# Kernel tuning notes

Hardware: AMD Instinct MI355X
Metric: run time of the kernel (lower is better)

The kernel has to match this reference:

```python
import jax, jax.numpy as jnp
import numpy as np

B, L, H = 8, 128, 768
VOCAB, FEAT_VOCAB, NUM_LABELS = 30522, 16384, 3


def setup_inputs() -> dict:
    key = jax.random.key(0)
    ks = jax.random.split(key, 12)
    return {
        "sequence_output": jax.random.normal(ks[0], (B, L, H), jnp.float32),
        "pooled_output": jax.random.normal(ks[1], (B, H), jnp.float32),
        "W_key": jax.random.normal(ks[2], (VOCAB, H), jnp.float32) * 0.02,
        "W_val": jax.random.normal(ks[3], (FEAT_VOCAB, H), jnp.float32) * 0.02,
        "W_dense": jax.random.normal(ks[4], (NUM_LABELS, 2 * H), jnp.float32) * 0.02,
        "b_dense": jnp.zeros((NUM_LABELS,), jnp.float32),
        "valid_ids": jax.random.randint(ks[5], (B, L), 0, 2, jnp.int32),
        "text_kv_indices": jax.random.randint(ks[6], (B, L), 0, VOCAB, jnp.int64 if jax.config.jax_enable_x64 else jnp.int32),
        "features": jax.random.randint(ks[7], (B, L, L), 0, FEAT_VOCAB, jnp.int64 if jax.config.jax_enable_x64 else jnp.int32),
        "pos_matrix": jax.random.randint(ks[8], (B, L, L), 0, 2, jnp.int32),
        "aspect_indices": jax.random.randint(ks[9], (B, L), 0, 2, jnp.int32),
    }


def reference(sequence_output, pooled_output, W_key, W_val, W_dense, b_dense,
              valid_ids, text_kv_indices, features, pos_matrix, aspect_indices):
    b, l, h = sequence_output.shape
    # --- vectorized valid-token pack (replaces per-sample python loop) ---
    # stable argsort puts valid (==1) token positions first, in order
    order = jnp.argsort(1 - valid_ids, axis=1, stable=True)          # [B,L]
    gathered = jnp.take_along_axis(sequence_output, order[:, :, None], axis=1)
    count = valid_ids.sum(axis=1)                                    # [B]
    keep = jnp.arange(l)[None, :] < count[:, None]                   # [B,L]
    valid_output = gathered * keep[:, :, None].astype(jnp.float32)
    asp = aspect_indices[:, :, None].astype(jnp.float32)             # [B,L,1]
    hidden = valid_output * asp
    # --- KeyValueMemoryNetwork ---
    Wk = W_key.at[0].set(0.0)   # padding_idx=0
    Wv = W_val.at[0].set(0.0)   # padding_idx=0
    key_embed = Wk[text_kv_indices]                                  # [B,L,H]
    value_embed = Wv[features]                                       # [B,L,L,H]
    scale = jnp.float32(np.power(h, 0.5))
    u = jnp.einsum('bqh,bkh->bqk', hidden, key_embed) / scale        # [B,L,L]
    delta = jnp.exp(u) * pos_matrix.astype(jnp.float32)
    p = delta / (delta.sum(axis=2, keepdims=True) + 1e-10)           # [B,L,L]
    o = jnp.einsum('bqk,bqkh->bqh', p, value_embed)                  # [B,L,H]
    aspect_len = (o != 0).sum(axis=1).astype(jnp.float32)            # [B,H]
    avg_o = o.sum(axis=1) / aspect_len                               # [B,H]
    # --- head (incro == 'cat'; dropout is identity at eval) ---
    c = jnp.concatenate([pooled_output, avg_o], axis=1)              # [B,2H]
    logits = c @ W_dense.T + b_dense                                 # [B,3]
    return logits
```

## Files before the change

### kernel.cpp

```cpp
#include <hip/hip_runtime.h>

#define NB 8
#define SL 128
#define HD 768

typedef float v2f __attribute__((ext_vector_type(2)));

__device__ __forceinline__ float bf_lo(unsigned int u) {
  return __uint_as_float(u << 16);
}
__device__ __forceinline__ float bf_hi(unsigned int u) {
  return __uint_as_float(u & 0xffff0000u);
}
__device__ __forceinline__ unsigned short f2bf(float x) {
  unsigned int b = __float_as_uint(x);
  b += 0x7fffu + ((b >> 16) & 1u);
  return (unsigned short)(b >> 16);
}

__global__ __launch_bounds__(256) void k_prep(
    const float* __restrict__ seq,
    const float* __restrict__ W_key,
    const float* __restrict__ W_val,
    const int* __restrict__ valid,
    const int* __restrict__ kvidx,
    const int* __restrict__ aspect,
    float* __restrict__ hidden,
    unsigned short* __restrict__ keyemb,
    unsigned int* __restrict__ wv8) {
  int blk = blockIdx.x;
  int tid = threadIdx.x;

  if (blk >= NB * SL) {
    int cb = blk - NB * SL;
    const float4* src = (const float4*)W_val;
    int base = cb * 1024 + tid;
#pragma unroll
    for (int it = 0; it < 4; ++it) {
      float4 v = src[base + 256 * it];
      int w = __builtin_amdgcn_cvt_pk_fp8_f32(v.x, v.y, 0, false);
      w = __builtin_amdgcn_cvt_pk_fp8_f32(v.z, v.w, w, true);
      wv8[base + 256 * it] = (unsigned int)w;
    }
    return;
  }

  int b = blk & 7;
  int i = blk >> 3;
  int bq = b * SL + i;
  int lane = tid & 63, wv = tid >> 6;

  __shared__ int s_wcnt[4];
  __shared__ int s_src;

  int v = (tid < SL) ? (valid[b * SL + tid] != 0) : 0;
  unsigned long long m = __ballot(v);
  if (lane == 0) s_wcnt[wv] = __popcll(m);
  if (tid == 0) s_src = SL;
  __syncthreads();
  int count = s_wcnt[0] + s_wcnt[1];
  if (v) {
    int rank = __popcll(m & ((1ull << lane) - 1ull)) + (wv == 1 ? s_wcnt[0] : 0);
    if (rank == i) s_src = tid;
  }
  __syncthreads();
  int src = s_src;

  if (tid < HD / 4) {
    float4 hv = make_float4(0.f, 0.f, 0.f, 0.f);
    if (i < count && src < SL) {
      float asp = (float)aspect[b * SL + i];
      const float4* srow = (const float4*)(seq + ((size_t)(b * SL + src)) * HD);
      float4 s = srow[tid];
      hv = make_float4(s.x * asp, s.y * asp, s.z * asp, s.w * asp);
    }
    ((float4*)(hidden + (size_t)bq * HD))[tid] = hv;

    int id = kvidx[b * SL + i];
    ushort4 kb = make_ushort4(0, 0, 0, 0);
    if (id != 0) {
      float4 kv = ((const float4*)(W_key + (size_t)id * HD))[tid];
      kb = make_ushort4(f2bf(kv.x), f2bf(kv.y), f2bf(kv.z), f2bf(kv.w));
    }
    ((ushort4*)(keyemb + (size_t)bq * HD))[tid] = kb;
  }
}

__global__ __launch_bounds__(512) void k_attend(
    const float* __restrict__ hidden,
    const unsigned short* __restrict__ keyemb,
    const int* __restrict__ features,
    const int* __restrict__ pos,
    const unsigned int* __restrict__ wv8,
    float* __restrict__ o) {
  int blk = blockIdx.x;
  int b = blk & 7;
  int q = blk >> 3;
  int bq = b * SL + q;
  int tid = threadIdx.x;
  int wave = tid >> 6, lane = tid & 63;

  __shared__ float s_p[SL];
  __shared__ int s_f[SL];
  __shared__ float s_pc[SL];
  __shared__ int s_fc[SL];
  __shared__ float s_o[8][HD];
  __shared__ float s_sum;
  __shared__ int s_cnt2[2];
  __shared__ int s_m;

  float4 hreg[3];
  {
    const float4* h4 = (const float4*)(hidden + (size_t)bq * HD);
#pragma unroll
    for (int j = 0; j < 3; ++j) hreg[j] = h4[lane + 64 * j];
  }
  if (tid < SL) s_f[tid] = features[(size_t)bq * SL + tid];

  const float rscale = 0.03608439182435161f;
  for (int k = wave; k < SL; k += 8) {
    const uint2* kr = (const uint2*)(keyemb + ((size_t)(b * SL + k)) * HD);
    float part = 0.f;
#pragma unroll
    for (int j = 0; j < 3; ++j) {
      uint2 kv = kr[lane + 64 * j];
      float4 h = hreg[j];
      part += bf_lo(kv.x) * h.x + bf_hi(kv.x) * h.y +
              bf_lo(kv.y) * h.z + bf_hi(kv.y) * h.w;
    }
#pragma unroll
    for (int off = 32; off; off >>= 1) part += __shfl_xor(part, off);
    if (lane == 0) s_p[k] = part * rscale;
  }
  __syncthreads();
  if (tid < SL) {
    float d = (pos[(size_t)bq * SL + tid] != 0) ? expf(s_p[tid]) : 0.f;
    s_p[tid] = d;
  }
  __syncthreads();
  if (tid < 64) {
    float part = s_p[tid] + s_p[tid + 64];
#pragma unroll
    for (int off = 32; off; off >>= 1) part += __shfl_xor(part, off);
    if (tid == 0) s_sum = part + 1e-10f;
  }
  __syncthreads();

  int keep = 0;
  float pv = 0.f;
  int fv = 0;
  if (tid < SL) {
    pv = s_p[tid] / s_sum;
    fv = s_f[tid];
    keep = (pv != 0.f) && (fv != 0);
  }
  unsigned long long km = __ballot(keep);
  if (lane == 0 && wave < 2) s_cnt2[wave] = __popcll(km);
  __syncthreads();
  if (keep) {
    int rank = __popcll(km & ((1ull << lane) - 1ull)) + (wave == 1 ? s_cnt2[0] : 0);
    s_pc[rank] = pv;
    s_fc[rank] = fv;
  }
  if (tid == 0) s_m = s_cnt2[0] + s_cnt2[1];
  __syncthreads();
  int mm = s_m;

  int niter = (mm + 15) >> 4;
  float myp = 0.f;
  int myf = 0;
  {
    int el = 2 * wave + 16 * (lane >> 1) + (lane & 1);
    if (lane < 16 && el < mm) { myp = s_pc[el]; myf = s_fc[el]; }
  }
  float4 a0 = make_float4(0.f, 0.f, 0.f, 0.f);
  float4 a1 = a0, a2 = a0;
  for (int j = 0; j < niter; ++j) {
    float pk0 = __shfl(myp, 2 * j);
    int f0 = __shfl(myf, 2 * j);
    float pk1 = __shfl(myp, 2 * j + 1);
    int f1 = __shfl(myf, 2 * j + 1);
    const unsigned int* vr0 = wv8 + (size_t)f0 * (HD / 4);
    const unsigned int* vr1 = wv8 + (size_t)f1 * (HD / 4);
    unsigned int x0 = vr0[lane], x1 = vr0[lane + 64], x2 = vr0[lane + 128];
    unsigned int y0 = vr1[lane], y1 = vr1[lane + 64], y2 = vr1[lane + 128];
    v2f p0, p1;
    p0 = __builtin_amdgcn_cvt_pk_f32_fp8(x0, false);
    p1 = __builtin_amdgcn_cvt_pk_f32_fp8(x0, true);
    a0.x += pk0 * p0.x; a0.y += pk0 * p0.y; a0.z += pk0 * p1.x; a0.w += pk0 * p1.y;
    p0 = __builtin_amdgcn_cvt_pk_f32_fp8(x1, false);
    p1 = __builtin_amdgcn_cvt_pk_f32_fp8(x1, true);
    a1.x += pk0 * p0.x; a1.y += pk0 * p0.y; a1.z += pk0 * p1.x; a1.w += pk0 * p1.y;
    p0 = __builtin_amdgcn_cvt_pk_f32_fp8(x2, false);
    p1 = __builtin_amdgcn_cvt_pk_f32_fp8(x2, true);
    a2.x += pk0 * p0.x; a2.y += pk0 * p0.y; a2.z += pk0 * p1.x; a2.w += pk0 * p1.y;
    p0 = __builtin_amdgcn_cvt_pk_f32_fp8(y0, false);
    p1 = __builtin_amdgcn_cvt_pk_f32_fp8(y0, true);
    a0.x += pk1 * p0.x; a0.y += pk1 * p0.y; a0.z += pk1 * p1.x; a0.w += pk1 * p1.y;
    p0 = __builtin_amdgcn_cvt_pk_f32_fp8(y1, false);
    p1 = __builtin_amdgcn_cvt_pk_f32_fp8(y1, true);
    a1.x += pk1 * p0.x; a1.y += pk1 * p0.y; a1.z += pk1 * p1.x; a1.w += pk1 * p1.y;
    p0 = __builtin_amdgcn_cvt_pk_f32_fp8(y2, false);
    p1 = __builtin_amdgcn_cvt_pk_f32_fp8(y2, true);
    a2.x += pk1 * p0.x; a2.y += pk1 * p0.y; a2.z += pk1 * p1.x; a2.w += pk1 * p1.y;
  }
  ((float4*)s_o[wave])[lane] = a0;
  ((float4*)s_o[wave])[lane + 64] = a1;
  ((float4*)s_o[wave])[lane + 128] = a2;
  __syncthreads();

  float* orow = o + (size_t)bq * HD;
  for (int h = tid; h < HD; h += 512) {
    float s = 0.f;
#pragma unroll
    for (int w = 0; w < 8; ++w) s += s_o[w][h];
    orow[h] = s;
  }
}

__global__ __launch_bounds__(512) void k_avg(
    const float* __restrict__ o, float* __restrict__ avg) {
  int b = blockIdx.x / 6, c = blockIdx.x % 6;
  int tid = threadIdx.x;
  int hc = tid & 127;
  int h = c * 128 + hc;
  int sub = tid >> 7;
  __shared__ float s_sum[4][128];
  __shared__ int s_cnt[4][128];
  float sum = 0.f;
  int cnt = 0;
#pragma unroll 8
  for (int q = sub * 32; q < (sub + 1) * 32; ++q) {
    float v = o[((size_t)(b * SL + q)) * HD + h];
    sum += v;
    cnt += (v != 0.f) ? 1 : 0;
  }
  s_sum[sub][hc] = sum;
  s_cnt[sub][hc] = cnt;
  __syncthreads();
  if (tid < 128) {
    float t = (s_sum[0][tid] + s_sum[1][tid]) + (s_sum[2][tid] + s_sum[3][tid]);
    int cc = (s_cnt[0][tid] + s_cnt[1][tid]) + (s_cnt[2][tid] + s_cnt[3][tid]);
    avg[(size_t)b * HD + c * 128 + tid] = t / (float)cc;
  }
}

__global__ __launch_bounds__(192) void k_dense(
    const float* __restrict__ pooled,
    const float* __restrict__ avg,
    const float* __restrict__ W_dense,
    const float* __restrict__ b_dense,
    float* __restrict__ out) {
  int b = blockIdx.x;
  int tid = threadIdx.x;
  int n = tid >> 6, lane = tid & 63;
  float part = 0.f;
  for (int j = lane; j < HD; j += 64)
    part += pooled[(size_t)b * HD + j] * W_dense[(size_t)n * (2 * HD) + j];
  for (int j = lane; j < HD; j += 64)
    part += avg[(size_t)b * HD + j] * W_dense[(size_t)n * (2 * HD) + HD + j];
#pragma unroll
  for (int off = 32; off; off >>= 1) part += __shfl_xor(part, off);
  if (lane == 0) out[b * 3 + n] = part + b_dense[n];
}

extern "C" void kernel_launch(void* const* d_in, const int* in_sizes, int n_in,
                              void* d_out, int out_size, void* d_ws, size_t ws_size,
                              hipStream_t stream) {
  const float* seq     = (const float*)d_in[0];
  const float* pooled  = (const float*)d_in[1];
  const float* W_key   = (const float*)d_in[2];
  const float* W_val   = (const float*)d_in[3];
  const float* W_dense = (const float*)d_in[4];
  const float* b_dense = (const float*)d_in[5];
  const int* valid     = (const int*)d_in[6];
  const int* kvidx     = (const int*)d_in[7];
  const int* features  = (const int*)d_in[8];
  const int* pos       = (const int*)d_in[9];
  const int* aspect    = (const int*)d_in[10];
  float* out = (float*)d_out;

  float* hidden = (float*)d_ws;
  unsigned short* keyemb =
      (unsigned short*)(hidden + (size_t)NB * SL * HD);
  float* o = (float*)(keyemb + (size_t)NB * SL * HD);
  float* avg = o + (size_t)NB * SL * HD;
  unsigned int* wv8 = (unsigned int*)(avg + (size_t)NB * HD);

  k_prep<<<NB * SL + 3072, 256, 0, stream>>>(seq, W_key, W_val, valid, kvidx,
                                             aspect, hidden, keyemb, wv8);
  k_attend<<<NB * SL, 512, 0, stream>>>(hidden, keyemb, features, pos, wv8, o);
  k_avg<<<NB * 6, 512, 0, stream>>>(o, avg);
  k_dense<<<NB, 192, 0, stream>>>(pooled, avg, W_dense, b_dense, out);
}
```

Before: 49.05 us.

## Store key embeddings as FP8 and widen value gather to 16-byte loads

Key embeddings are now converted to FP8 instead of bf16, which halves the bytes read in the attention score loop. The value aggregation loop also changes: each wave handles four packed entries per iteration using uint4 loads. Only 48 lanes are active, and the padded shared arrays are zeroed so the tail entries contribute nothing. This cuts global traffic and shuffle overhead, at the cost of lower precision in the attention logits and idle lanes.

```diff
diff --git a/kernel.cpp b/kernel.cpp
--- a/kernel.cpp
+++ b/kernel.cpp
@@ -3,20 +3,9 @@
 #define NB 8
 #define SL 128
 #define HD 768
+#define HDU (HD / 4)
 
 typedef float v2f __attribute__((ext_vector_type(2)));
-
-__device__ __forceinline__ float bf_lo(unsigned int u) {
-  return __uint_as_float(u << 16);
-}
-__device__ __forceinline__ float bf_hi(unsigned int u) {
-  return __uint_as_float(u & 0xffff0000u);
-}
-__device__ __forceinline__ unsigned short f2bf(float x) {
-  unsigned int b = __float_as_uint(x);
-  b += 0x7fffu + ((b >> 16) & 1u);
-  return (unsigned short)(b >> 16);
-}
 
 __global__ __launch_bounds__(256) void k_prep(
     const float* __restrict__ seq,
@@ -26,7 +15,7 @@
     const int* __restrict__ kvidx,
     const int* __restrict__ aspect,
     float* __restrict__ hidden,
-    unsigned short* __restrict__ keyemb,
+    unsigned int* __restrict__ keyemb,
     unsigned int* __restrict__ wv8) {
   int blk = blockIdx.x;
   int tid = threadIdx.x;
@@ -77,18 +66,20 @@
     ((float4*)(hidden + (size_t)bq * HD))[tid] = hv;
 
     int id = kvidx[b * SL + i];
-    ushort4 kb = make_ushort4(0, 0, 0, 0);
+    unsigned int kb = 0;
     if (id != 0) {
       float4 kv = ((const float4*)(W_key + (size_t)id * HD))[tid];
-      kb = make_ushort4(f2bf(kv.x), f2bf(kv.y), f2bf(kv.z), f2bf(kv.w));
-    }
-    ((ushort4*)(keyemb + (size_t)bq * HD))[tid] = kb;
+      int w = __builtin_amdgcn_cvt_pk_fp8_f32(kv.x, kv.y, 0, false);
+      w = __builtin_amdgcn_cvt_pk_fp8_f32(kv.z, kv.w, w, true);
+      kb = (unsigned int)w;
+    }
+    keyemb[(size_t)bq * HDU + tid] = kb;
   }
 }
 
 __global__ __launch_bounds__(512) void k_attend(
     const float* __restrict__ hidden,
-    const unsigned short* __restrict__ keyemb,
+    const unsigned int* __restrict__ keyemb,
     const int* __restrict__ features,
     const int* __restrict__ pos,
     const unsigned int* __restrict__ wv8,
@@ -102,13 +93,18 @@
 
   __shared__ float s_p[SL];
   __shared__ int s_f[SL];
-  __shared__ float s_pc[SL];
-  __shared__ int s_fc[SL];
+  __shared__ __align__(16) float s_pc[SL + 32];
+  __shared__ __align__(16) int s_fc[SL + 32];
   __shared__ float s_o[8][HD];
   __shared__ float s_sum;
   __shared__ int s_cnt2[2];
   __shared__ int s_m;
 
+  if (tid < SL + 32) {
+    s_pc[tid] = 0.f;
+    s_fc[tid] = 0;
+  }
+
   float4 hreg[3];
   {
     const float4* h4 = (const float4*)(hidden + (size_t)bq * HD);
@@ -119,14 +115,15 @@
 
   const float rscale = 0.03608439182435161f;
   for (int k = wave; k < SL; k += 8) {
-    const uint2* kr = (const uint2*)(keyemb + ((size_t)(b * SL + k)) * HD);
+    const unsigned int* kr = keyemb + (size_t)(b * SL + k) * HDU;
     float part = 0.f;
 #pragma unroll
     for (int j = 0; j < 3; ++j) {
-      uint2 kv = kr[lane + 64 * j];
+      unsigned int kv = kr[lane + 64 * j];
       float4 h = hreg[j];
-      part += bf_lo(kv.x) * h.x + bf_hi(kv.x) * h.y +
-              bf_lo(kv.y) * h.z + bf_hi(kv.y) * h.w;
+      v2f p0 = __builtin_amdgcn_cvt_pk_f32_fp8(kv, false);
+      v2f p1 = __builtin_amdgcn_cvt_pk_f32_fp8(kv, true);
+      part += p0.x * h.x + p0.y * h.y + p1.x * h.z + p1.y * h.w;
     }
 #pragma unroll
     for (int off = 32; off; off >>= 1) part += __shfl_xor(part, off);
@@ -166,47 +163,43 @@
   __syncthreads();
   int mm = s_m;
 
-  int niter = (mm + 15) >> 4;
-  float myp = 0.f;
-  int myf = 0;
-  {
-    int el = 2 * wave + 16 * (lane >> 1) + (lane & 1);
-    if (lane < 16 && el < mm) { myp = s_pc[el]; myf = s_fc[el]; }
-  }
-  float4 a0 = make_float4(0.f, 0.f, 0.f, 0.f);
-  float4 a1 = a0, a2 = a0;
+  int niter = (mm + 31) >> 5;
+  float4 acc[4];
+#pragma unroll
+  for (int c = 0; c < 4; ++c) acc[c] = make_float4(0.f, 0.f, 0.f, 0.f);
+
   for (int j = 0; j < niter; ++j) {
-    float pk0 = __shfl(myp, 2 * j);
-    int f0 = __shfl(myf, 2 * j);
-    float pk1 = __shfl(myp, 2 * j + 1);
-    int f1 = __shfl(myf, 2 * j + 1);
-    const unsigned int* vr0 = wv8 + (size_t)f0 * (HD / 4);
-    const unsigned int* vr1 = wv8 + (size_t)f1 * (HD / 4);
-    unsigned int x0 = vr0[lane], x1 = vr0[lane + 64], x2 = vr0[lane + 128];
-    unsigned int y0 = vr1[lane], y1 = vr1[lane + 64], y2 = vr1[lane + 128];
-    v2f p0, p1;
-    p0 = __builtin_amdgcn_cvt_pk_f32_fp8(x0, false);
-    p1 = __builtin_amdgcn_cvt_pk_f32_fp8(x0, true);
-    a0.x += pk0 * p0.x; a0.y += pk0 * p0.y; a0.z += pk0 * p1.x; a0.w += pk0 * p1.y;
-    p0 = __builtin_amdgcn_cvt_pk_f32_fp8(x1, false);
-    p1 = __builtin_amdgcn_cvt_pk_f32_fp8(x1, true);
-    a1.x += pk0 * p0.x; a1.y += pk0 * p0.y; a1.z += pk0 * p1.x; a1.w += pk0 * p1.y;
-    p0 = __builtin_amdgcn_cvt_pk_f32_fp8(x2, false);
-    p1 = __builtin_amdgcn_cvt_pk_f32_fp8(x2, true);
-    a2.x += pk0 * p0.x; a2.y += pk0 * p0.y; a2.z += pk0 * p1.x; a2.w += pk0 * p1.y;
-    p0 = __builtin_amdgcn_cvt_pk_f32_fp8(y0, false);
-    p1 = __builtin_amdgcn_cvt_pk_f32_fp8(y0, true);
-    a0.x += pk1 * p0.x; a0.y += pk1 * p0.y; a0.z += pk1 * p1.x; a0.w += pk1 * p1.y;
-    p0 = __builtin_amdgcn_cvt_pk_f32_fp8(y1, false);
-    p1 = __builtin_amdgcn_cvt_pk_f32_fp8(y1, true);
-    a1.x += pk1 * p0.x; a1.y += pk1 * p0.y; a1.z += pk1 * p1.x; a1.w += pk1 * p1.y;
-    p0 = __builtin_amdgcn_cvt_pk_f32_fp8(y2, false);
-    p1 = __builtin_amdgcn_cvt_pk_f32_fp8(y2, true);
-    a2.x += pk1 * p0.x; a2.y += pk1 * p0.y; a2.z += pk1 * p1.x; a2.w += pk1 * p1.y;
-  }
-  ((float4*)s_o[wave])[lane] = a0;
-  ((float4*)s_o[wave])[lane + 64] = a1;
-  ((float4*)s_o[wave])[lane + 128] = a2;
+    int eb = 32 * j + 4 * wave;
+    float4 pk4 = *(const float4*)&s_pc[eb];
+    int4 f4 = *(const int4*)&s_fc[eb];
+    if (lane < 48) {
+      uint4 x0 = ((const uint4*)(wv8 + (size_t)f4.x * HDU))[lane];
+      uint4 x1 = ((const uint4*)(wv8 + (size_t)f4.y * HDU))[lane];
+      uint4 x2 = ((const uint4*)(wv8 + (size_t)f4.z * HDU))[lane];
+      uint4 x3 = ((const uint4*)(wv8 + (size_t)f4.w * HDU))[lane];
+#define ACC_U(U, PK, C)                                              \
+  {                                                                  \
+    v2f p0 = __builtin_amdgcn_cvt_pk_f32_fp8((U), false);            \
+    v2f p1 = __builtin_amdgcn_cvt_pk_f32_fp8((U), true);             \
+    acc[C].x += (PK)*p0.x;                                           \
+    acc[C].y += (PK)*p0.y;                                           \
+    acc[C].z += (PK)*p1.x;                                           \
+    acc[C].w += (PK)*p1.y;                                           \
+  }
+#define ACC_ROW(X, PK) \
+  ACC_U(X.x, PK, 0) ACC_U(X.y, PK, 1) ACC_U(X.z, PK, 2) ACC_U(X.w, PK, 3)
+      ACC_ROW(x0, pk4.x)
+      ACC_ROW(x1, pk4.y)
+      ACC_ROW(x2, pk4.z)
+      ACC_ROW(x3, pk4.w)
+#undef ACC_ROW
+#undef ACC_U
+    }
+  }
+  if (lane < 48) {
+#pragma unroll
+    for (int c = 0; c < 4; ++c) ((float4*)s_o[wave])[4 * lane + c] = acc[c];
+  }
   __syncthreads();
 
   float* orow = o + (size_t)bq * HD;
@@ -281,9 +274,9 @@
   float* out = (float*)d_out;
 
   float* hidden = (float*)d_ws;
-  unsigned short* keyemb =
-      (unsigned short*)(hidden + (size_t)NB * SL * HD);
-  float* o = (float*)(keyemb + (size_t)NB * SL * HD);
+  unsigned int* keyemb =
+      (unsigned int*)(hidden + (size_t)NB * SL * HD);
+  float* o = (float*)(keyemb + (size_t)NB * SL * HDU);
   float* avg = o + (size_t)NB * SL * HD;
   unsigned int* wv8 = (unsigned int*)(avg + (size_t)NB * HD);
 
```

After: 55.05 us. 12.2% more time.

## Fuse sequence averaging into attend via atomics and store key embeddings as fp8

Applied to the files above, without the earlier changes.

Removes the k_avg kernel and the full o buffer. Each attend block now atomically adds its output row and its nonzero count into per-batch sum/count arrays, which k_prep zeroes with extra blocks. k_dense divides sum by count itself. Key embeddings are also stored as fp8 instead of bf16, halving key traffic at the cost of precision in the attention logits. Atomic contention is 128 adds per address and float atomic ordering becomes nondeterministic.

```diff
diff --git a/kernel.cpp b/kernel.cpp
--- a/kernel.cpp
+++ b/kernel.cpp
@@ -3,20 +3,9 @@
 #define NB 8
 #define SL 128
 #define HD 768
+#define HDU (HD / 4)
 
 typedef float v2f __attribute__((ext_vector_type(2)));
-
-__device__ __forceinline__ float bf_lo(unsigned int u) {
-  return __uint_as_float(u << 16);
-}
-__device__ __forceinline__ float bf_hi(unsigned int u) {
-  return __uint_as_float(u & 0xffff0000u);
-}
-__device__ __forceinline__ unsigned short f2bf(float x) {
-  unsigned int b = __float_as_uint(x);
-  b += 0x7fffu + ((b >> 16) & 1u);
-  return (unsigned short)(b >> 16);
-}
 
 __global__ __launch_bounds__(256) void k_prep(
     const float* __restrict__ seq,
@@ -26,11 +15,18 @@
     const int* __restrict__ kvidx,
     const int* __restrict__ aspect,
     float* __restrict__ hidden,
-    unsigned short* __restrict__ keyemb,
-    unsigned int* __restrict__ wv8) {
+    unsigned int* __restrict__ keyemb,
+    unsigned int* __restrict__ wv8,
+    unsigned int* __restrict__ avg_zero) {
   int blk = blockIdx.x;
   int tid = threadIdx.x;
 
+  if (blk >= NB * SL + 3072) {
+    int base = (blk - NB * SL - 3072) * 2048 + tid;
+#pragma unroll
+    for (int it = 0; it < 8; ++it) avg_zero[base + 256 * it] = 0u;
+    return;
+  }
   if (blk >= NB * SL) {
     int cb = blk - NB * SL;
     const float4* src = (const float4*)W_val;
@@ -77,22 +73,25 @@
     ((float4*)(hidden + (size_t)bq * HD))[tid] = hv;
 
     int id = kvidx[b * SL + i];
-    ushort4 kb = make_ushort4(0, 0, 0, 0);
+    unsigned int kb = 0;
     if (id != 0) {
       float4 kv = ((const float4*)(W_key + (size_t)id * HD))[tid];
-      kb = make_ushort4(f2bf(kv.x), f2bf(kv.y), f2bf(kv.z), f2bf(kv.w));
-    }
-    ((ushort4*)(keyemb + (size_t)bq * HD))[tid] = kb;
+      int w = __builtin_amdgcn_cvt_pk_fp8_f32(kv.x, kv.y, 0, false);
+      w = __builtin_amdgcn_cvt_pk_fp8_f32(kv.z, kv.w, w, true);
+      kb = (unsigned int)w;
+    }
+    keyemb[(size_t)bq * HDU + tid] = kb;
   }
 }
 
 __global__ __launch_bounds__(512) void k_attend(
     const float* __restrict__ hidden,
-    const unsigned short* __restrict__ keyemb,
+    const unsigned int* __restrict__ keyemb,
     const int* __restrict__ features,
     const int* __restrict__ pos,
     const unsigned int* __restrict__ wv8,
-    float* __restrict__ o) {
+    float* __restrict__ avg_sum,
+    int* __restrict__ avg_cnt) {
   int blk = blockIdx.x;
   int b = blk & 7;
   int q = blk >> 3;
@@ -119,14 +118,15 @@
 
   const float rscale = 0.03608439182435161f;
   for (int k = wave; k < SL; k += 8) {
-    const uint2* kr = (const uint2*)(keyemb + ((size_t)(b * SL + k)) * HD);
+    const unsigned int* kr = keyemb + (size_t)(b * SL + k) * HDU;
     float part = 0.f;
 #pragma unroll
     for (int j = 0; j < 3; ++j) {
-      uint2 kv = kr[lane + 64 * j];
+      unsigned int kv = kr[lane + 64 * j];
       float4 h = hreg[j];
-      part += bf_lo(kv.x) * h.x + bf_hi(kv.x) * h.y +
-              bf_lo(kv.y) * h.z + bf_hi(kv.y) * h.w;
+      v2f p0 = __builtin_amdgcn_cvt_pk_f32_fp8(kv, false);
+      v2f p1 = __builtin_amdgcn_cvt_pk_f32_fp8(kv, true);
+      part += p0.x * h.x + p0.y * h.y + p1.x * h.z + p1.y * h.w;
     }
 #pragma unroll
     for (int off = 32; off; off >>= 1) part += __shfl_xor(part, off);
@@ -180,8 +180,8 @@
     int f0 = __shfl(myf, 2 * j);
     float pk1 = __shfl(myp, 2 * j + 1);
     int f1 = __shfl(myf, 2 * j + 1);
-    const unsigned int* vr0 = wv8 + (size_t)f0 * (HD / 4);
-    const unsigned int* vr1 = wv8 + (size_t)f1 * (HD / 4);
+    const unsigned int* vr0 = wv8 + (size_t)f0 * HDU;
+    const unsigned int* vr1 = wv8 + (size_t)f1 * HDU;
     unsigned int x0 = vr0[lane], x1 = vr0[lane + 64], x2 = vr0[lane + 128];
     unsigned int y0 = vr1[lane], y1 = vr1[lane + 64], y2 = vr1[lane + 128];
     v2f p0, p1;
@@ -209,56 +209,34 @@
   ((float4*)s_o[wave])[lane + 128] = a2;
   __syncthreads();
 
-  float* orow = o + (size_t)bq * HD;
   for (int h = tid; h < HD; h += 512) {
     float s = 0.f;
 #pragma unroll
     for (int w = 0; w < 8; ++w) s += s_o[w][h];
-    orow[h] = s;
-  }
-}
-
-__global__ __launch_bounds__(512) void k_avg(
-    const float* __restrict__ o, float* __restrict__ avg) {
-  int b = blockIdx.x / 6, c = blockIdx.x % 6;
-  int tid = threadIdx.x;
-  int hc = tid & 127;
-  int h = c * 128 + hc;
-  int sub = tid >> 7;
-  __shared__ float s_sum[4][128];
-  __shared__ int s_cnt[4][128];
-  float sum = 0.f;
-  int cnt = 0;
-#pragma unroll 8
-  for (int q = sub * 32; q < (sub + 1) * 32; ++q) {
-    float v = o[((size_t)(b * SL + q)) * HD + h];
-    sum += v;
-    cnt += (v != 0.f) ? 1 : 0;
-  }
-  s_sum[sub][hc] = sum;
-  s_cnt[sub][hc] = cnt;
-  __syncthreads();
-  if (tid < 128) {
-    float t = (s_sum[0][tid] + s_sum[1][tid]) + (s_sum[2][tid] + s_sum[3][tid]);
-    int cc = (s_cnt[0][tid] + s_cnt[1][tid]) + (s_cnt[2][tid] + s_cnt[3][tid]);
-    avg[(size_t)b * HD + c * 128 + tid] = t / (float)cc;
+    atomicAdd(&avg_sum[(size_t)b * HD + h], s);
+    atomicAdd(&avg_cnt[(size_t)b * HD + h], (s != 0.f) ? 1 : 0);
   }
 }
 
 __global__ __launch_bounds__(192) void k_dense(
     const float* __restrict__ pooled,
-    const float* __restrict__ avg,
+    const float* __restrict__ avg_sum,
+    const int* __restrict__ avg_cnt,
     const float* __restrict__ W_dense,
     const float* __restrict__ b_dense,
     float* __restrict__ out) {
   int b = blockIdx.x;
   int tid = threadIdx.x;
+  __shared__ float s_avg[HD];
+  for (int c = tid; c < HD; c += 192)
+    s_avg[c] = avg_sum[(size_t)b * HD + c] / (float)avg_cnt[(size_t)b * HD + c];
+  __syncthreads();
   int n = tid >> 6, lane = tid & 63;
   float part = 0.f;
   for (int j = lane; j < HD; j += 64)
     part += pooled[(size_t)b * HD + j] * W_dense[(size_t)n * (2 * HD) + j];
   for (int j = lane; j < HD; j += 64)
-    part += avg[(size_t)b * HD + j] * W_dense[(size_t)n * (2 * HD) + HD + j];
+    part += s_avg[j] * W_dense[(size_t)n * (2 * HD) + HD + j];
 #pragma unroll
   for (int off = 32; off; off >>= 1) part += __shfl_xor(part, off);
   if (lane == 0) out[b * 3 + n] = part + b_dense[n];
@@ -281,15 +259,16 @@
   float* out = (float*)d_out;
 
   float* hidden = (float*)d_ws;
-  unsigned short* keyemb =
-      (unsigned short*)(hidden + (size_t)NB * SL * HD);
-  float* o = (float*)(keyemb + (size_t)NB * SL * HD);
-  float* avg = o + (size_t)NB * SL * HD;
-  unsigned int* wv8 = (unsigned int*)(avg + (size_t)NB * HD);
-
-  k_prep<<<NB * SL + 3072, 256, 0, stream>>>(seq, W_key, W_val, valid, kvidx,
-                                             aspect, hidden, keyemb, wv8);
-  k_attend<<<NB * SL, 512, 0, stream>>>(hidden, keyemb, features, pos, wv8, o);
-  k_avg<<<NB * 6, 512, 0, stream>>>(o, avg);
-  k_dense<<<NB, 192, 0, stream>>>(pooled, avg, W_dense, b_dense, out);
-}
+  unsigned int* keyemb =
+      (unsigned int*)(hidden + (size_t)NB * SL * HD);
+  float* avg_sum = (float*)(keyemb + (size_t)NB * SL * HDU);
+  int* avg_cnt = (int*)(avg_sum + (size_t)NB * HD);
+  unsigned int* wv8 = (unsigned int*)(avg_cnt + (size_t)NB * HD);
+
+  k_prep<<<NB * SL + 3072 + 6, 256, 0, stream>>>(
+      seq, W_key, W_val, valid, kvidx, aspect, hidden, keyemb, wv8,
+      (unsigned int*)avg_sum);
+  k_attend<<<NB * SL, 512, 0, stream>>>(hidden, keyemb, features, pos, wv8,
+                                        avg_sum, avg_cnt);
+  k_dense<<<NB, 192, 0, stream>>>(pooled, avg_sum, avg_cnt, W_dense, b_dense, out);
+}
```

Result: no change. 48.46 us, median of 6 (-1.2%).
